# Performance work log

Hardware: AMD Instinct MI355X
Metric: run time of the kernel (lower is better)

Reference implementation:

```python
import jax, jax.numpy as jnp
import numpy as np

N_HEADS = 8


def setup_inputs() -> dict:
    key = jax.random.key(0)
    ks = jax.random.split(key, 12)
    B, C, H, W = 16, 256, 64, 64
    std = 1.0 / np.sqrt(C)  # init_std(conv) ~ 1/sqrt(fan_in) for a 1x1 conv
    return {
        "x": jax.random.normal(ks[0], (B, C, H, W), jnp.float32),
        "mod_multiplier": jax.random.normal(ks[1], (B, C), jnp.float32),
        "mod_bias": jax.random.normal(ks[2], (B, C), jnp.float32),
        "qkv_w": jax.random.normal(ks[3], (3 * C, C), jnp.float32) * std,
        "qkv_b": jnp.zeros((3 * C,), jnp.float32),
        "pe_q_h": jax.random.normal(ks[4], (1, C, H, 1), jnp.float32) * 0.02,
        "pe_q_w": jax.random.normal(ks[5], (1, C, 1, W), jnp.float32) * 0.02,
        "pe_k_h": jax.random.normal(ks[6], (1, C, H, 1), jnp.float32) * 0.02,
        "pe_k_w": jax.random.normal(ks[7], (1, C, 1, W), jnp.float32) * 0.02,
        "pre_act_bias": jnp.zeros((1, C, 1, 1), jnp.float32),
        "pre_qkv_bias": jnp.zeros((1, C, 1, 1), jnp.float32),
    }


def reference(x, mod_multiplier, mod_bias, qkv_w, qkv_b, pe_q_h, pe_q_w, pe_k_h, pe_k_w, pre_act_bias, pre_qkv_bias):
    B, C, H, W = x.shape
    hs = C // N_HEADS  # head_size
    dot_scale = jnp.asarray(hs, x.dtype) ** 0.5

    x_preact = jax.nn.silu(x + pre_act_bias)
    # 1x1 conv == channel GEMM: [B,C,H,W] x [3C,C] -> [B,3C,H,W]
    qkv = jnp.einsum('bchw,oc->bohw', x_preact + pre_qkv_bias, qkv_w) + qkv_b[None, :, None, None]
    q, k, v = jnp.split(qkv, 3, axis=1)

    q = q + pe_q_h + pe_q_w
    k = k + pe_k_h + pe_k_w
    q = q * mod_multiplier[:, :, None, None] + mod_bias[:, :, None, None]

    # view as [B, n_heads, head_size, H*W]
    q = q.reshape(B, N_HEADS, hs, H * W)
    k = k.reshape(B, N_HEADS, hs, H * W)
    v = v.reshape(B, N_HEADS, hs, H * W)

    # channel-attention: logits [B, n_heads, hs, hs]
    logits = jnp.einsum('bhcn,bhdn->bhcd', q, k) / dot_scale
    weights = jax.nn.softmax(logits, axis=-1)
    out = jnp.einsum('bhcd,bhdn->bhcn', weights, v).reshape(B, C, H, W)

    return jnp.concatenate((x_preact, out), axis=1)
```

## Files before the change

kernel.cpp:

```cpp
#include <hip/hip_runtime.h>

typedef short bf16x8 __attribute__((ext_vector_type(8)));
typedef float f32x4 __attribute__((ext_vector_type(4)));

__device__ __forceinline__ float b2f(unsigned short u) {
  union { unsigned int i; float f; } v; v.i = ((unsigned int)u) << 16; return v.f;
}
__device__ __forceinline__ unsigned short f2b(float f) {
  unsigned int u = __float_as_uint(f);
  u += 0x7fffu + ((u >> 16) & 1u);
  return (unsigned short)(u >> 16);
}
__device__ __forceinline__ float silu_f(float s) { return s / (1.0f + __expf(-s)); }

__device__ __forceinline__ void split2(float f, unsigned short& h, unsigned short& l) {
  h = f2b(f);
  l = f2b(f - b2f(h));
}

__device__ __forceinline__ void gload16(const unsigned short* g, unsigned short* l) {
  __builtin_amdgcn_global_load_lds(
      (const __attribute__((address_space(1))) unsigned int*)g,
      (__attribute__((address_space(3))) unsigned int*)l, 16, 0, 0);
}

__device__ __forceinline__ void unpack8(const unsigned* p, bf16x8& hi, bf16x8& lo) {
  uint4 a = *(const uint4*)p;
  uint4 b = *(const uint4*)(p + 4);
  unsigned u[8] = {a.x, a.y, a.z, a.w, b.x, b.y, b.z, b.w};
  unsigned hw[4], lw[4];
  #pragma unroll
  for (int j = 0; j < 4; j++) {
    hw[j] = __builtin_amdgcn_perm(u[2 * j + 1], u[2 * j], 0x05040100u);
    lw[j] = __builtin_amdgcn_perm(u[2 * j + 1], u[2 * j], 0x07060302u);
  }
  hi = *(bf16x8*)hw;
  lo = *(bf16x8*)lw;
}

__global__ __launch_bounds__(256) void k_wsplit(
    const float* __restrict__ W, unsigned short* __restrict__ Wh,
    unsigned short* __restrict__ Wl) {
  int e = (blockIdx.x * 256 + threadIdx.x) * 8;
  float4 a = *(const float4*)(W + e);
  float4 b = *(const float4*)(W + e + 4);
  float v[8] = {a.x, a.y, a.z, a.w, b.x, b.y, b.z, b.w};
  unsigned short h[8], l[8];
  #pragma unroll
  for (int j = 0; j < 8; j++) split2(v[j], h[j], l[j]);
  uint4 ph, pl;
  ph.x = h[0] | ((unsigned)h[1] << 16); ph.y = h[2] | ((unsigned)h[3] << 16);
  ph.z = h[4] | ((unsigned)h[5] << 16); ph.w = h[6] | ((unsigned)h[7] << 16);
  pl.x = l[0] | ((unsigned)l[1] << 16); pl.y = l[2] | ((unsigned)l[3] << 16);
  pl.z = l[4] | ((unsigned)l[5] << 16); pl.w = l[6] | ((unsigned)l[7] << 16);
  *(uint4*)(Wh + e) = ph;
  *(uint4*)(Wl + e) = pl;
}

__global__ __launch_bounds__(256) void k_prep(
    const float* __restrict__ x, const float* __restrict__ pab,
    const float* __restrict__ pqb, float* __restrict__ out) {
  __shared__ unsigned short th[64 * 64], tl[64 * 64];
  int blk = blockIdx.x;
  int nb = blk & 63;
  int cb = (blk >> 6) & 3;
  int b = blk >> 8;
  int n0 = nb * 64, c0 = cb * 64;
  int t = threadIdx.x;
  int nn = (t & 15) * 4;
  #pragma unroll
  for (int p = 0; p < 2; p++) {
    int c = 2 * (p * 16 + (t >> 4));
    float pa0 = pab[c0 + c], pq0 = pqb[c0 + c];
    float pa1 = pab[c0 + c + 1], pq1 = pqb[c0 + c + 1];
    float4 x0 = *(const float4*)(x + ((long long)(b * 256 + c0 + c)) * 4096 + n0 + nn);
    float4 x1 = *(const float4*)(x + ((long long)(b * 256 + c0 + c + 1)) * 4096 + n0 + nn);
    float s0[4] = {silu_f(x0.x + pa0), silu_f(x0.y + pa0),
                   silu_f(x0.z + pa0), silu_f(x0.w + pa0)};
    float s1[4] = {silu_f(x1.x + pa1), silu_f(x1.y + pa1),
                   silu_f(x1.z + pa1), silu_f(x1.w + pa1)};
    float4 sv0 = {s0[0], s0[1], s0[2], s0[3]};
    float4 sv1 = {s1[0], s1[1], s1[2], s1[3]};
    *(float4*)(out + ((long long)(b * 512 + c0 + c)) * 4096 + n0 + nn) = sv0;
    *(float4*)(out + ((long long)(b * 512 + c0 + c + 1)) * 4096 + n0 + nn) = sv1;
    float t0[4] = {s0[0] + pq0, s0[1] + pq0, s0[2] + pq0, s0[3] + pq0};
    float t1[4] = {s1[0] + pq1, s1[1] + pq1, s1[2] + pq1, s1[3] + pq1};
    #pragma unroll
    for (int j = 0; j < 4; j++) {
      int nr = nn + j;
      unsigned short h0, l0, h1, l1;
      split2(t0[j], h0, l0);
      split2(t1[j], h1, l1);
      int pcol = ((((c >> 3) ^ (nr & 7)) << 3) | (c & 7));
      *(unsigned int*)(th + nr * 64 + pcol) = (unsigned)h0 | ((unsigned)h1 << 16);
      *(unsigned int*)(tl + nr * 64 + pcol) = (unsigned)l0 | ((unsigned)l1 << 16);
    }
  }
  __syncthreads();
  unsigned short* Th = (unsigned short*)(out + ((long long)(b * 512 + 256)) * 4096);
  unsigned short* Tl = Th + 4096 * 256;
  #pragma unroll
  for (int q = 0; q < 2; q++) {
    int s = q * 256 + t;
    int n = s >> 3, sc = s & 7;
    int psc = sc ^ (n & 7);
    uint4 vh = *(const uint4*)(th + n * 64 + psc * 8);
    uint4 vl = *(const uint4*)(tl + n * 64 + psc * 8);
    *(uint4*)(Th + (long long)(n0 + n) * 256 + c0 + sc * 8) = vh;
    *(uint4*)(Tl + (long long)(n0 + n) * 256 + c0 + sc * 8) = vl;
  }
}

__global__ __launch_bounds__(256) void k_qkl(
    const unsigned short* __restrict__ Wh, const unsigned short* __restrict__ Wl,
    const float* __restrict__ qkvb,
    const float* __restrict__ peqh, const float* __restrict__ peqw,
    const float* __restrict__ pekh, const float* __restrict__ pekw,
    const float* __restrict__ modm, const float* __restrict__ modb,
    const float* __restrict__ outT, float* __restrict__ logits) {
  __shared__ __align__(16) unsigned short stg[12288];
  __shared__ __align__(16) unsigned qk[64 * 128];
  int bx = blockIdx.x;
  int ntile = bx & 31, h = (bx >> 5) & 7, b = bx >> 8;
  int n0 = ntile * 128;
  int t = threadIdx.x, lane = t & 63, w = t >> 6;
  int l15 = lane & 15, l4 = lane >> 4;

  const unsigned short* Th =
      (const unsigned short*)(outT + ((long long)(b * 512 + 256)) * 4096);
  const unsigned short* Tl = Th + 4096 * 256;

  const unsigned short* csrc[6];
  unsigned short* cdst[6];
  int lrow = lane >> 2;
  int lslot = ((lane & 3) ^ ((lane >> 3) & 3)) * 8;
  #pragma unroll
  for (int i = 0; i < 6; i++) {
    int c = w * 6 + i;
    const unsigned short* plane;
    int rowb, ldsoff;
    if (c < 8) {
      plane = (c & 4) ? Wl : Wh;
      int sub = c & 3;
      rowb = h * 32 + ((sub & 2) ? 256 : 0) + (sub & 1) * 16;
      ldsoff = c * 512;
    } else {
      int ci = c - 8;
      plane = (ci & 8) ? Tl : Th;
      rowb = n0 + (ci & 7) * 16;
      ldsoff = 4096 + ci * 512;
    }
    csrc[i] = plane + (long long)(rowb + lrow) * 256 + lslot;
    cdst[i] = stg + ldsoff;
  }

  int sw = (l4 ^ ((l15 >> 1) & 3)) << 3;
  f32x4 z = {0.f, 0.f, 0.f, 0.f};
  f32x4 acc[4][2];
  #pragma unroll
  for (int i = 0; i < 4; i++)
    #pragma unroll
    for (int j = 0; j < 2; j++) acc[i][j] = z;

  for (int step = 0; step < 8; ++step) {
    int k0 = step * 32;
    #pragma unroll
    for (int i = 0; i < 6; i++) gload16(csrc[i] + k0, cdst[i]);
    __syncthreads();
    bf16x8 ah[4], al[4], bh[2], bl[2];
    #pragma unroll
    for (int i = 0; i < 4; i++) {
      int ro = (i * 16 + l15) * 32 + sw;
      ah[i] = *(const bf16x8*)(stg + ro);
      al[i] = *(const bf16x8*)(stg + 2048 + ro);
    }
    #pragma unroll
    for (int j = 0; j < 2; j++) {
      int ro = (w * 32 + j * 16 + l15) * 32 + sw;
      bh[j] = *(const bf16x8*)(stg + 4096 + ro);
      bl[j] = *(const bf16x8*)(stg + 8192 + ro);
    }
    #pragma unroll
    for (int i = 0; i < 4; i++)
      #pragma unroll
      for (int j = 0; j < 2; j++) {
        acc[i][j] = __builtin_amdgcn_mfma_f32_16x16x32_bf16(ah[i], bh[j], acc[i][j], 0, 0, 0);
        acc[i][j] = __builtin_amdgcn_mfma_f32_16x16x32_bf16(ah[i], bl[j], acc[i][j], 0, 0, 0);
        acc[i][j] = __builtin_amdgcn_mfma_f32_16x16x32_bf16(al[i], bh[j], acc[i][j], 0, 0, 0);
      }
    __syncthreads();
  }

  int b256 = b * 256;
  #pragma unroll
  for (int i = 0; i < 4; i++) {
    #pragma unroll
    for (int r = 0; r < 4; r++) {
      int row = i * 16 + l4 * 4 + r;
      int cch = h * 32 + (row & 31);
      float bias = qkvb[(row & 32) ? (256 + cch) : cch];
      float mm = 0.f, mb = 0.f;
      if (row < 32) { mm = modm[b256 + cch]; mb = modb[b256 + cch]; }
      #pragma unroll
      for (int j = 0; j < 2; j++) {
        int nl = w * 32 + j * 16 + l15;
        int n = n0 + nl;
        int hh = n >> 6, ww = n & 63;
        float v = acc[i][j][r] + bias;
        if (row < 32) {
          v += peqh[cch * 64 + hh] + peqw[cch * 64 + ww];
          v = v * mm + mb;
        } else {
          v += pekh[cch * 64 + hh] + pekw[cch * 64 + ww];
        }
        unsigned short hi_, lo_;
        split2(v, hi_, lo_);
        int pch = (nl >> 3) ^ (row & 15);
        qk[row * 128 + pch * 8 + (nl & 7)] = (unsigned)hi_ | ((unsigned)lo_ << 16);
      }
    }
  }
  __syncthreads();

  f32x4 acc2[2][2] = {z, z, z, z};
  int chn = w * 4 + l4;
  bf16x8 qh[2], ql[2], kh[2], kl[2];
  #pragma unroll
  for (int i2 = 0; i2 < 2; i2++) {
    int row = i2 * 16 + l15;
    unpack8(qk + row * 128 + ((chn ^ l15) << 3), qh[i2], ql[i2]);
    unpack8(qk + (row + 32) * 128 + ((chn ^ l15) << 3), kh[i2], kl[i2]);
  }
  acc2[0][0] = __builtin_amdgcn_mfma_f32_16x16x32_bf16(qh[0], kh[0], acc2[0][0], 0, 0, 0);
  acc2[0][0] = __builtin_amdgcn_mfma_f32_16x16x32_bf16(qh[0], kl[0], acc2[0][0], 0, 0, 0);
  acc2[0][0] = __builtin_amdgcn_mfma_f32_16x16x32_bf16(ql[0], kh[0], acc2[0][0], 0, 0, 0);
  acc2[0][1] = __builtin_amdgcn_mfma_f32_16x16x32_bf16(qh[0], kh[1], acc2[0][1], 0, 0, 0);
  acc2[0][1] = __builtin_amdgcn_mfma_f32_16x16x32_bf16(qh[0], kl[1], acc2[0][1], 0, 0, 0);
  acc2[0][1] = __builtin_amdgcn_mfma_f32_16x16x32_bf16(ql[0], kh[1], acc2[0][1], 0, 0, 0);
  acc2[1][0] = __builtin_amdgcn_mfma_f32_16x16x32_bf16(qh[1], kh[0], acc2[1][0], 0, 0, 0);
  acc2[1][0] = __builtin_amdgcn_mfma_f32_16x16x32_bf16(qh[1], kl[0], acc2[1][0], 0, 0, 0);
  acc2[1][0] = __builtin_amdgcn_mfma_f32_16x16x32_bf16(ql[1], kh[0], acc2[1][0], 0, 0, 0);
  acc2[1][1] = __builtin_amdgcn_mfma_f32_16x16x32_bf16(qh[1], kh[1], acc2[1][1], 0, 0, 0);
  acc2[1][1] = __builtin_amdgcn_mfma_f32_16x16x32_bf16(qh[1], kl[1], acc2[1][1], 0, 0, 0);
  acc2[1][1] = __builtin_amdgcn_mfma_f32_16x16x32_bf16(ql[1], kh[1], acc2[1][1], 0, 0, 0);

  float* red = (float*)stg;
  #pragma unroll
  for (int i2 = 0; i2 < 2; i2++)
    #pragma unroll
    for (int j2 = 0; j2 < 2; j2++)
      #pragma unroll
      for (int r = 0; r < 4; r++)
        red[w * 1024 + (i2 * 16 + l4 * 4 + r) * 32 + j2 * 16 + l15] = acc2[i2][j2][r];
  __syncthreads();
  const float scale = 0.1767766952966369f;
  int bhid = b * 8 + h;
  #pragma unroll
  for (int i = 0; i < 4; i++) {
    int idx = i * 256 + t;
    float s = (red[idx] + red[1024 + idx] + red[2048 + idx] + red[3072 + idx]) * scale;
    atomicAdd(logits + (long long)bhid * 1024 + idx, s);
  }
}

template <int USE_LO>
__global__ __launch_bounds__(512, 4) void k_qkv(
    const unsigned short* __restrict__ Wh, const unsigned short* __restrict__ Wl,
    const float* __restrict__ qkvb,
    const float* __restrict__ peqh, const float* __restrict__ peqw,
    const float* __restrict__ pekh, const float* __restrict__ pekw,
    const float* __restrict__ modm, const float* __restrict__ modb,
    float* __restrict__ out, float* __restrict__ kv,
    int o_base, int obt) {
  extern __shared__ unsigned short sm[];
  const int BUFS = USE_LO ? 16384 : 8192;

  int bx = blockIdx.x;
  int nb = bx & 31;
  int hb = bx >> 5;
  int ob = hb % obt;
  int b = hb / obt;
  int o0 = o_base + ob * 128, n0 = nb * 128;
  int t = threadIdx.x;
  int lane = t & 63, w = t >> 6;
  int wm = w >> 2, wn = w & 3;
  int l15 = lane & 15, l4 = lane >> 4;

  const unsigned short* Th =
      (const unsigned short*)(out + ((long long)(b * 512 + 256)) * 4096);
  const unsigned short* Tl = Th + 4096 * 256;

  const unsigned short* src;
  int dstoff, row0;
  if (USE_LO) {
    int p = w >> 1, hh = w & 1;
    src = (p == 0) ? Wh : (p == 1) ? Wl : (p == 2) ? Th : Tl;
    row0 = ((p < 2) ? o0 : n0) + hh * 64;
    dstoff = p * 4096 + hh * 2048;
  } else {
    int p = w >> 2, qq = w & 3;
    src = (p == 0) ? Wh : Th;
    row0 = ((p == 0) ? o0 : n0) + qq * 32;
    dstoff = p * 4096 + qq * 1024;
  }
  const int nI = USE_LO ? 4 : 2;
  int laneoff = (lane >> 2) * 256 + (((lane & 3) ^ ((lane >> 3) & 3)) << 3);
  const unsigned short* sbase = src + (long long)row0 * 256 + laneoff;

  f32x4 z = {0.f, 0.f, 0.f, 0.f};
  f32x4 acc[4][2];
  #pragma unroll
  for (int i = 0; i < 4; i++)
    #pragma unroll
    for (int j = 0; j < 2; j++) acc[i][j] = z;

  int sw = (l4 ^ ((l15 >> 1) & 3)) << 3;

  #pragma unroll
  for (int i = 0; i < nI; i++) gload16(sbase + i * 4096, sm + dstoff + i * 512);

  int cur = 0;
  for (int step = 0; step < 8; ++step) {
    if (step < 7) {
      const unsigned short* sp = sbase + (step + 1) * 32;
      unsigned short* dp = sm + (cur ^ 1) * BUFS + dstoff;
      #pragma unroll
      for (int i = 0; i < nI; i++) gload16(sp + i * 4096, dp + i * 512);
      if (USE_LO) asm volatile("s_waitcnt vmcnt(4)" ::: "memory");
      else        asm volatile("s_waitcnt vmcnt(2)" ::: "memory");
    } else {
      asm volatile("s_waitcnt vmcnt(0)" ::: "memory");
    }
    __builtin_amdgcn_s_barrier();
    __builtin_amdgcn_sched_barrier(0);
    unsigned short* Ah = sm + cur * BUFS;
    unsigned short* Al = Ah + 4096;
    unsigned short* Bh = Ah + (USE_LO ? 8192 : 4096);
    unsigned short* Bl = Ah + 12288;
    bf16x8 ah[4], al[4], bh[2], bl[2];
    #pragma unroll
    for (int i = 0; i < 4; i++) {
      int rowA = (wm * 64 + i * 16 + l15) * 32;
      ah[i] = *(const bf16x8*)(Ah + rowA + sw);
      if (USE_LO) al[i] = *(const bf16x8*)(Al + rowA + sw);
    }
    #pragma unroll
    for (int j = 0; j < 2; j++) {
      int rowB = (wn * 32 + j * 16 + l15) * 32;
      bh[j] = *(const bf16x8*)(Bh + rowB + sw);
      if (USE_LO) bl[j] = *(const bf16x8*)(Bl + rowB + sw);
    }
    #pragma unroll
    for (int i = 0; i < 4; i++)
      #pragma unroll
      for (int j = 0; j < 2; j++) {
        acc[i][j] = __builtin_amdgcn_mfma_f32_16x16x32_bf16(ah[i], bh[j], acc[i][j], 0, 0, 0);
        if (USE_LO) {
          acc[i][j] = __builtin_amdgcn_mfma_f32_16x16x32_bf16(ah[i], bl[j], acc[i][j], 0, 0, 0);
          acc[i][j] = __builtin_amdgcn_mfma_f32_16x16x32_bf16(al[i], bh[j], acc[i][j], 0, 0, 0);
        }
      }
    __builtin_amdgcn_sched_barrier(0);
    __builtin_amdgcn_s_barrier();
    cur ^= 1;
  }

  int part = o0 >> 8;
  #pragma unroll
  for (int i = 0; i < 4; i++) {
    #pragma unroll
    for (int r = 0; r < 4; r++) {
      int o = o0 + wm * 64 + i * 16 + l4 * 4 + r;
      int cch = o & 255;
      float bias = qkvb[o];
      float mm = 0.f, mb = 0.f;
      if (part == 0) { mm = modm[b * 256 + cch]; mb = modb[b * 256 + cch]; }
      #pragma unroll
      for (int j = 0; j < 2; j++) {
        int n = n0 + wn * 32 + j * 16 + l15;
        float v = acc[i][j][r] + bias;
        int hh = n >> 6, ww = n & 63;
        if (part == 0) {
          v += peqh[cch * 64 + hh] + peqw[cch * 64 + ww];
          v = v * mm + mb;
          unsigned short h, l; split2(v, h, l);
          ((unsigned*)out)[((long long)(b * 512 + cch)) * 4096 + n] =
              (unsigned)h | ((unsigned)l << 16);
        } else if (part == 1) {
          v += pekh[cch * 64 + hh] + pekw[cch * 64 + ww];
          unsigned short h, l; split2(v, h, l);
          ((unsigned*)kv)[((long long)(b * 256 + cch)) * 4096 + n] =
              (unsigned)h | ((unsigned)l << 16);
        } else {
          kv[((long long)(b * 256 + cch)) * 4096 + n] = v;
        }
      }
    }
  }
}

__global__ __launch_bounds__(256) void k_pv(
    const float* __restrict__ kv,
    const float* __restrict__ logits,
    float* __restrict__ out) {
  int bx = blockIdx.x;
  int ntile = bx & 15, bh = bx >> 4;
  int b = bh >> 3, h = bh & 7;
  int t = threadIdx.x;
  __shared__ float raw[32][33];
  __shared__ float wsm[32][33];
  #pragma unroll
  for (int i = 0; i < 4; i++) {
    int idx = i * 256 + t;
    raw[idx >> 5][idx & 31] = logits[(long long)bh * 1024 + idx];
  }
  __syncthreads();
  if (t < 32) {
    float mx = -1e30f;
    for (int d = 0; d < 32; d++) mx = fmaxf(mx, raw[t][d]);
    float e[32]; float s = 0.f;
    for (int d = 0; d < 32; d++) { e[d] = __expf(raw[t][d] - mx); s += e[d]; }
    float inv = 1.0f / s;
    for (int d = 0; d < 32; d++) wsm[t][d] = e[d] * inv;
  }
  __syncthreads();
  int rg = t >> 6;
  int nl = (t & 63) * 4;
  int n0 = ntile * 256 + nl;
  const float* vb = kv + ((long long)(b * 256 + h * 32)) * 4096 + n0;
  float acc[8][4];
  #pragma unroll
  for (int r = 0; r < 8; r++)
    #pragma unroll
    for (int i = 0; i < 4; i++) acc[r][i] = 0.f;
  for (int d = 0; d < 32; d++) {
    float4 vv = *(const float4*)(vb + (long long)d * 4096);
    #pragma unroll
    for (int r = 0; r < 8; r++) {
      float wv = wsm[rg * 8 + r][d];
      acc[r][0] += wv * vv.x; acc[r][1] += wv * vv.y;
      acc[r][2] += wv * vv.z; acc[r][3] += wv * vv.w;
    }
  }
  #pragma unroll
  for (int r = 0; r < 8; r++) {
    long long oidx = ((long long)(b * 512 + 256 + h * 32 + rg * 8 + r)) * 4096 + n0;
    float4 ov = {acc[r][0], acc[r][1], acc[r][2], acc[r][3]};
    *(float4*)(out + oidx) = ov;
  }
}

extern "C" void kernel_launch(void* const* d_in, const int* in_sizes, int n_in,
                              void* d_out, int out_size, void* d_ws, size_t ws_size,
                              hipStream_t stream) {
  const float* x    = (const float*)d_in[0];
  const float* modm = (const float*)d_in[1];
  const float* modb = (const float*)d_in[2];
  const float* Wq   = (const float*)d_in[3];
  const float* qkvb = (const float*)d_in[4];
  const float* peqh = (const float*)d_in[5];
  const float* peqw = (const float*)d_in[6];
  const float* pekh = (const float*)d_in[7];
  const float* pekw = (const float*)d_in[8];
  const float* pab  = (const float*)d_in[9];
  const float* pqb  = (const float*)d_in[10];
  float* out = (float*)d_out;

  unsigned short* Wh = (unsigned short*)d_ws;
  unsigned short* Wl = Wh + 768 * 256;
  float* logits = (float*)((char*)d_ws + (1 << 20));
  float* kv = (float*)((char*)d_ws + 3 * (1 << 20));

  hipMemsetAsync(logits, 0, 16 * 8 * 32 * 32 * sizeof(float), stream);
  k_wsplit<<<96, 256, 0, stream>>>(Wq, Wh, Wl);
  k_prep<<<4096, 256, 0, stream>>>(x, pab, pqb, out);
  k_qkl<<<4096, 256, 0, stream>>>(Wh, Wl, qkvb, peqh, peqw, pekh, pekw,
                                  modm, modb, out, logits);
  k_qkv<0><<<1024, 512, 32768, stream>>>(Wh, Wl, qkvb, peqh, peqw, pekh, pekw,
                                         modm, modb, out, kv, 512, 2);
  k_pv<<<2048, 256, 0, stream>>>(kv, logits, out);
}
```

Before: 347.6 us.

## Fuse V projection GEMM into Q/K logits kernel, dropping separate k_qkv launch

The V-part of the 1x1-conv projection (rows 512..767 of W, hi-only bf16) is now computed inside k_qkl, reusing the already-staged activation tiles in LDS, and written to kv directly. The separate k_qkv launch, which reloaded the activation planes from global memory, is removed. LDS is unified into one 32KB buffer shared by staging, qk and reduction, with an added barrier, and launch bounds request 3 blocks per CU. This trades an extra load slice and MFMAs per step in k_qkl for eliminating a full second pass over the activations.

```diff
diff --git a/kernel.cpp b/kernel.cpp
--- a/kernel.cpp
+++ b/kernel.cpp
@@ -111,15 +111,19 @@
   }
 }
 
-__global__ __launch_bounds__(256) void k_qkl(
+__global__ __launch_bounds__(256, 3) void k_qkl(
     const unsigned short* __restrict__ Wh, const unsigned short* __restrict__ Wl,
     const float* __restrict__ qkvb,
     const float* __restrict__ peqh, const float* __restrict__ peqw,
     const float* __restrict__ pekh, const float* __restrict__ pekw,
     const float* __restrict__ modm, const float* __restrict__ modb,
-    const float* __restrict__ outT, float* __restrict__ logits) {
-  __shared__ __align__(16) unsigned short stg[12288];
-  __shared__ __align__(16) unsigned qk[64 * 128];
+    const float* __restrict__ outT, float* __restrict__ kv,
+    float* __restrict__ logits) {
+  __shared__ __align__(16) unsigned char smem[32768];
+  unsigned short* stg = (unsigned short*)smem;
+  unsigned* qk = (unsigned*)smem;
+  float* red = (float*)smem;
+
   int bx = blockIdx.x;
   int ntile = bx & 31, h = (bx >> 5) & 7, b = bx >> 8;
   int n0 = ntile * 128;
@@ -130,25 +134,33 @@
       (const unsigned short*)(outT + ((long long)(b * 512 + 256)) * 4096);
   const unsigned short* Tl = Th + 4096 * 256;
 
-  const unsigned short* csrc[6];
-  unsigned short* cdst[6];
+  const unsigned short* csrc[7];
+  unsigned short* cdst[7];
+  int nc = (w < 2) ? 7 : 6;
   int lrow = lane >> 2;
   int lslot = ((lane & 3) ^ ((lane >> 3) & 3)) * 8;
   #pragma unroll
-  for (int i = 0; i < 6; i++) {
-    int c = w * 6 + i;
+  for (int i = 0; i < 7; i++) {
+    int c = w + 4 * i;
+    if (c > 25) c = 25;
     const unsigned short* plane;
     int rowb, ldsoff;
-    if (c < 8) {
-      plane = (c & 4) ? Wl : Wh;
-      int sub = c & 3;
-      rowb = h * 32 + ((sub & 2) ? 256 : 0) + (sub & 1) * 16;
+    if (c < 4) {
+      plane = Wh; rowb = ((c & 2) ? 256 : 0) + h * 32 + (c & 1) * 16;
       ldsoff = c * 512;
+    } else if (c < 8) {
+      int s2 = c - 4;
+      plane = Wl; rowb = ((s2 & 2) ? 256 : 0) + h * 32 + (s2 & 1) * 16;
+      ldsoff = c * 512;
+    } else if (c < 10) {
+      plane = Wh; rowb = 512 + h * 32 + (c - 8) * 16;
+      ldsoff = 4096 + (c - 8) * 512;
+    } else if (c < 18) {
+      plane = Th; rowb = n0 + (c - 10) * 16;
+      ldsoff = 5120 + (c - 10) * 512;
     } else {
-      int ci = c - 8;
-      plane = (ci & 8) ? Tl : Th;
-      rowb = n0 + (ci & 7) * 16;
-      ldsoff = 4096 + ci * 512;
+      plane = Tl; rowb = n0 + (c - 18) * 16;
+      ldsoff = 9216 + (c - 18) * 512;
     }
     csrc[i] = plane + (long long)(rowb + lrow) * 256 + lslot;
     cdst[i] = stg + ldsoff;
@@ -157,17 +169,36 @@
   int sw = (l4 ^ ((l15 >> 1) & 3)) << 3;
   f32x4 z = {0.f, 0.f, 0.f, 0.f};
   f32x4 acc[4][2];
+  f32x4 accv[2][2];
   #pragma unroll
   for (int i = 0; i < 4; i++)
     #pragma unroll
     for (int j = 0; j < 2; j++) acc[i][j] = z;
+  #pragma unroll
+  for (int i = 0; i < 2; i++)
+    #pragma unroll
+    for (int j = 0; j < 2; j++) accv[i][j] = z;
 
   for (int step = 0; step < 8; ++step) {
     int k0 = step * 32;
     #pragma unroll
-    for (int i = 0; i < 6; i++) gload16(csrc[i] + k0, cdst[i]);
+    for (int i = 0; i < 7; i++)
+      if (i < nc) gload16(csrc[i] + k0, cdst[i]);
     __syncthreads();
-    bf16x8 ah[4], al[4], bh[2], bl[2];
+    bf16x8 bh[2], av[2];
+    #pragma unroll
+    for (int j = 0; j < 2; j++)
+      bh[j] = *(const bf16x8*)(stg + 5120 + (w * 32 + j * 16 + l15) * 32 + sw);
+    #pragma unroll
+    for (int i = 0; i < 2; i++)
+      av[i] = *(const bf16x8*)(stg + 4096 + (i * 16 + l15) * 32 + sw);
+    #pragma unroll
+    for (int i = 0; i < 2; i++)
+      #pragma unroll
+      for (int j = 0; j < 2; j++)
+        accv[i][j] = __builtin_amdgcn_mfma_f32_16x16x32_bf16(av[i], bh[j], accv[i][j], 0, 0, 0);
+    __builtin_amdgcn_sched_barrier(0);
+    bf16x8 ah[4], al[4], bl[2];
     #pragma unroll
     for (int i = 0; i < 4; i++) {
       int ro = (i * 16 + l15) * 32 + sw;
@@ -175,11 +206,8 @@
       al[i] = *(const bf16x8*)(stg + 2048 + ro);
     }
     #pragma unroll
-    for (int j = 0; j < 2; j++) {
-      int ro = (w * 32 + j * 16 + l15) * 32 + sw;
-      bh[j] = *(const bf16x8*)(stg + 4096 + ro);
-      bl[j] = *(const bf16x8*)(stg + 8192 + ro);
-    }
+    for (int j = 0; j < 2; j++)
+      bl[j] = *(const bf16x8*)(stg + 9216 + (w * 32 + j * 16 + l15) * 32 + sw);
     #pragma unroll
     for (int i = 0; i < 4; i++)
       #pragma unroll
@@ -192,6 +220,21 @@
   }
 
   int b256 = b * 256;
+  #pragma unroll
+  for (int i = 0; i < 2; i++) {
+    #pragma unroll
+    for (int r = 0; r < 4; r++) {
+      int row = i * 16 + l4 * 4 + r;
+      int cch = h * 32 + row;
+      float bias = qkvb[512 + cch];
+      #pragma unroll
+      for (int j = 0; j < 2; j++) {
+        int n = n0 + w * 32 + j * 16 + l15;
+        kv[((long long)(b256 + cch)) * 4096 + n] = accv[i][j][r] + bias;
+      }
+    }
+  }
+
   #pragma unroll
   for (int i = 0; i < 4; i++) {
     #pragma unroll
@@ -244,7 +287,7 @@
   acc2[1][1] = __builtin_amdgcn_mfma_f32_16x16x32_bf16(qh[1], kl[1], acc2[1][1], 0, 0, 0);
   acc2[1][1] = __builtin_amdgcn_mfma_f32_16x16x32_bf16(ql[1], kh[1], acc2[1][1], 0, 0, 0);
 
-  float* red = (float*)stg;
+  __syncthreads();
   #pragma unroll
   for (int i2 = 0; i2 < 2; i2++)
     #pragma unroll
@@ -260,142 +303,6 @@
     int idx = i * 256 + t;
     float s = (red[idx] + red[1024 + idx] + red[2048 + idx] + red[3072 + idx]) * scale;
     atomicAdd(logits + (long long)bhid * 1024 + idx, s);
-  }
-}
-
-template <int USE_LO>
-__global__ __launch_bounds__(512, 4) void k_qkv(
-    const unsigned short* __restrict__ Wh, const unsigned short* __restrict__ Wl,
-    const float* __restrict__ qkvb,
-    const float* __restrict__ peqh, const float* __restrict__ peqw,
-    const float* __restrict__ pekh, const float* __restrict__ pekw,
-    const float* __restrict__ modm, const float* __restrict__ modb,
-    float* __restrict__ out, float* __restrict__ kv,
-    int o_base, int obt) {
-  extern __shared__ unsigned short sm[];
-  const int BUFS = USE_LO ? 16384 : 8192;
-
-  int bx = blockIdx.x;
-  int nb = bx & 31;
-  int hb = bx >> 5;
-  int ob = hb % obt;
-  int b = hb / obt;
-  int o0 = o_base + ob * 128, n0 = nb * 128;
-  int t = threadIdx.x;
-  int lane = t & 63, w = t >> 6;
-  int wm = w >> 2, wn = w & 3;
-  int l15 = lane & 15, l4 = lane >> 4;
-
-  const unsigned short* Th =
-      (const unsigned short*)(out + ((long long)(b * 512 + 256)) * 4096);
-  const unsigned short* Tl = Th + 4096 * 256;
-
-  const unsigned short* src;
-  int dstoff, row0;
-  if (USE_LO) {
-    int p = w >> 1, hh = w & 1;
-    src = (p == 0) ? Wh : (p == 1) ? Wl : (p == 2) ? Th : Tl;
-    row0 = ((p < 2) ? o0 : n0) + hh * 64;
-    dstoff = p * 4096 + hh * 2048;
-  } else {
-    int p = w >> 2, qq = w & 3;
-    src = (p == 0) ? Wh : Th;
-    row0 = ((p == 0) ? o0 : n0) + qq * 32;
-    dstoff = p * 4096 + qq * 1024;
-  }
-  const int nI = USE_LO ? 4 : 2;
-  int laneoff = (lane >> 2) * 256 + (((lane & 3) ^ ((lane >> 3) & 3)) << 3);
-  const unsigned short* sbase = src + (long long)row0 * 256 + laneoff;
-
-  f32x4 z = {0.f, 0.f, 0.f, 0.f};
-  f32x4 acc[4][2];
-  #pragma unroll
-  for (int i = 0; i < 4; i++)
-    #pragma unroll
-    for (int j = 0; j < 2; j++) acc[i][j] = z;
-
-  int sw = (l4 ^ ((l15 >> 1) & 3)) << 3;
-
-  #pragma unroll
-  for (int i = 0; i < nI; i++) gload16(sbase + i * 4096, sm + dstoff + i * 512);
-
-  int cur = 0;
-  for (int step = 0; step < 8; ++step) {
-    if (step < 7) {
-      const unsigned short* sp = sbase + (step + 1) * 32;
-      unsigned short* dp = sm + (cur ^ 1) * BUFS + dstoff;
-      #pragma unroll
-      for (int i = 0; i < nI; i++) gload16(sp + i * 4096, dp + i * 512);
-      if (USE_LO) asm volatile("s_waitcnt vmcnt(4)" ::: "memory");
-      else        asm volatile("s_waitcnt vmcnt(2)" ::: "memory");
-    } else {
-      asm volatile("s_waitcnt vmcnt(0)" ::: "memory");
-    }
-    __builtin_amdgcn_s_barrier();
-    __builtin_amdgcn_sched_barrier(0);
-    unsigned short* Ah = sm + cur * BUFS;
-    unsigned short* Al = Ah + 4096;
-    unsigned short* Bh = Ah + (USE_LO ? 8192 : 4096);
-    unsigned short* Bl = Ah + 12288;
-    bf16x8 ah[4], al[4], bh[2], bl[2];
-    #pragma unroll
-    for (int i = 0; i < 4; i++) {
-      int rowA = (wm * 64 + i * 16 + l15) * 32;
-      ah[i] = *(const bf16x8*)(Ah + rowA + sw);
-      if (USE_LO) al[i] = *(const bf16x8*)(Al + rowA + sw);
-    }
-    #pragma unroll
-    for (int j = 0; j < 2; j++) {
-      int rowB = (wn * 32 + j * 16 + l15) * 32;
-      bh[j] = *(const bf16x8*)(Bh + rowB + sw);
-      if (USE_LO) bl[j] = *(const bf16x8*)(Bl + rowB + sw);
-    }
-    #pragma unroll
-    for (int i = 0; i < 4; i++)
-      #pragma unroll
-      for (int j = 0; j < 2; j++) {
-        acc[i][j] = __builtin_amdgcn_mfma_f32_16x16x32_bf16(ah[i], bh[j], acc[i][j], 0, 0, 0);
-        if (USE_LO) {
-          acc[i][j] = __builtin_amdgcn_mfma_f32_16x16x32_bf16(ah[i], bl[j], acc[i][j], 0, 0, 0);
-          acc[i][j] = __builtin_amdgcn_mfma_f32_16x16x32_bf16(al[i], bh[j], acc[i][j], 0, 0, 0);
-        }
-      }
-    __builtin_amdgcn_sched_barrier(0);
-    __builtin_amdgcn_s_barrier();
-    cur ^= 1;
-  }
-
-  int part = o0 >> 8;
-  #pragma unroll
-  for (int i = 0; i < 4; i++) {
-    #pragma unroll
-    for (int r = 0; r < 4; r++) {
-      int o = o0 + wm * 64 + i * 16 + l4 * 4 + r;
-      int cch = o & 255;
-      float bias = qkvb[o];
-      float mm = 0.f, mb = 0.f;
-      if (part == 0) { mm = modm[b * 256 + cch]; mb = modb[b * 256 + cch]; }
-      #pragma unroll
-      for (int j = 0; j < 2; j++) {
-        int n = n0 + wn * 32 + j * 16 + l15;
-        float v = acc[i][j][r] + bias;
-        int hh = n >> 6, ww = n & 63;
-        if (part == 0) {
-          v += peqh[cch * 64 + hh] + peqw[cch * 64 + ww];
-          v = v * mm + mb;
-          unsigned short h, l; split2(v, h, l);
-          ((unsigned*)out)[((long long)(b * 512 + cch)) * 4096 + n] =
-              (unsigned)h | ((unsigned)l << 16);
-        } else if (part == 1) {
-          v += pekh[cch * 64 + hh] + pekw[cch * 64 + ww];
-          unsigned short h, l; split2(v, h, l);
-          ((unsigned*)kv)[((long long)(b * 256 + cch)) * 4096 + n] =
-              (unsigned)h | ((unsigned)l << 16);
-        } else {
-          kv[((long long)(b * 256 + cch)) * 4096 + n] = v;
-        }
-      }
-    }
   }
 }
 
@@ -475,8 +382,6 @@
   k_wsplit<<<96, 256, 0, stream>>>(Wq, Wh, Wl);
   k_prep<<<4096, 256, 0, stream>>>(x, pab, pqb, out);
   k_qkl<<<4096, 256, 0, stream>>>(Wh, Wl, qkvb, peqh, peqw, pekh, pekw,
-                                  modm, modb, out, logits);
-  k_qkv<0><<<1024, 512, 32768, stream>>>(Wh, Wl, qkvb, peqh, peqw, pekh, pekw,
-                                         modm, modb, out, kv, 512, 2);
+                                  modm, modb, out, kv, logits);
   k_pv<<<2048, 256, 0, stream>>>(kv, logits, out);
 }
```

Result: faster. 317.6 us (-8.6%).
